# Kernel optimization log

Hardware: AMD Instinct MI355X
Metric: run time of the kernel (lower is better)

Reference implementation:

```python
import jax, jax.numpy as jnp
import numpy as np

N = 50000
E = 800000
IN_FEAT = 128
HEADS = 2
HEAD_DIM = 64  # hidden_feat // num_heads for 'concat'
HIDDEN = HEADS * HEAD_DIM
N_CLASSES = 16
NEG_SLOPE = 0.2
BN_EPS = 1e-5


def setup_inputs() -> dict:
    key = jax.random.key(0)
    ks = jax.random.split(key, 20)
    s = 0.1  # weight scale for numerical sanity
    return {
        "x": jax.random.normal(ks[0], (N, IN_FEAT), jnp.float32),
        "src0": jax.random.randint(ks[1], (E,), 0, N, jnp.int32),
        "dst0": jax.random.randint(ks[2], (E,), 0, N, jnp.int32),
        "ew0": jax.random.uniform(ks[3], (E,), jnp.float32),
        "src1": jax.random.randint(ks[4], (E,), 0, N, jnp.int32),
        "dst1": jax.random.randint(ks[5], (E,), 0, N, jnp.int32),
        "ew1": jax.random.uniform(ks[6], (E,), jnp.float32),
        "fc_w0": jax.random.normal(ks[7], (HIDDEN, IN_FEAT), jnp.float32) * s,
        "bias0": jnp.zeros((HIDDEN,), jnp.float32),
        "attn_l0": jax.random.normal(ks[8], (HEADS, HEAD_DIM), jnp.float32) * s,
        "attn_r0": jax.random.normal(ks[9], (HEADS, HEAD_DIM), jnp.float32) * s,
        "fc_w1": jax.random.normal(ks[10], (HIDDEN, IN_FEAT), jnp.float32) * s,
        "bias1": jnp.zeros((HIDDEN,), jnp.float32),
        "attn_l1": jax.random.normal(ks[11], (HEADS, HEAD_DIM), jnp.float32) * s,
        "attn_r1": jax.random.normal(ks[12], (HEADS, HEAD_DIM), jnp.float32) * s,
        "skip_w": jax.random.normal(ks[13], (HIDDEN, IN_FEAT), jnp.float32) * s,
        "skip_b": jnp.zeros((HIDDEN,), jnp.float32),
        "bn_gamma": jnp.ones((HIDDEN,), jnp.float32),
        "bn_beta": jnp.zeros((HIDDEN,), jnp.float32),
        "clf_w": jax.random.normal(ks[14], (N_CLASSES, HIDDEN), jnp.float32) * s,
        "clf_b": jnp.zeros((N_CLASSES,), jnp.float32),
    }


def _weighted_gat(x, src, dst, ew, fc_w, bias, attn_l, attn_r):
    # DGL GATConv with per-edge weight scaling of attention.
    f = (x @ fc_w.T).reshape(N, HEADS, HEAD_DIM)          # [N,H,D]
    el = jnp.sum(f * attn_l, axis=-1)                      # [N,H]
    er = jnp.sum(f * attn_r, axis=-1)                      # [N,H]
    e = jax.nn.leaky_relu(el[src] + er[dst], NEG_SLOPE)    # [E,H]
    # edge softmax over incoming edges of each dst, numerically stable
    m = jax.ops.segment_max(e, dst, num_segments=N)        # [N,H]
    ex = jnp.exp(e - m[dst])
    den = jax.ops.segment_sum(ex, dst, num_segments=N)     # [N,H]
    alpha = ex / den[dst]                                  # [E,H]
    alpha = alpha * ew[:, None]                            # edge-weight scaling
    msg = alpha[..., None] * f[src]                        # [E,H,D]
    out = jax.ops.segment_sum(msg, dst, num_segments=N)    # [N,H,D]
    return out + bias.reshape(1, HEADS, HEAD_DIM)


def reference(x, src0, dst0, ew0, src1, dst1, ew1,
              fc_w0, bias0, attn_l0, attn_r0,
              fc_w1, bias1, attn_l1, attn_r1,
              skip_w, skip_b, bn_gamma, bn_beta, clf_w, clf_b):
    # HeteroGraphConv with aggregate='sum': sum per-relation GAT outputs
    h2 = _weighted_gat(x, src0, dst0, ew0, fc_w0, bias0, attn_l0, attn_r0) \
       + _weighted_gat(x, src1, dst1, ew1, fc_w1, bias1, attn_l1, attn_r1)
    # multihead 'concat' aggregate with relu: flatten heads
    h2 = jax.nn.relu(h2).reshape(N, HIDDEN)
    # linear skip + residual add (dropout is identity at eval)
    h = (x @ skip_w.T + skip_b) + h2
    # classifier: BatchNorm1d (batch stats) -> ReLU -> Linear
    mu = jnp.mean(h, axis=0)
    var = jnp.mean((h - mu) ** 2, axis=0)
    hn = (h - mu) * jax.lax.rsqrt(var + BN_EPS) * bn_gamma + bn_beta
    logits = jax.nn.relu(hn) @ clf_w.T + clf_b
    return logits
```

## Files before the change

### kernel.cpp

```cpp
#include <hip/hip_runtime.h>
#include <hip/hip_bf16.h>

#define N_NODES 50000
#define N_EDGES 800000
#define HID 128
#define NEG_SLOPE 0.2f
#define BN_EPS 1e-5f

#define NBLK 256
#define BINSZ 512
#define BINSH 9
#define NBINS 98

typedef __bf16 v8bf __attribute__((ext_vector_type(8)));
typedef float v4f __attribute__((ext_vector_type(4)));

__device__ __forceinline__ float leaky(float v) {
    return (v > 0.f) ? v : v * NEG_SLOPE;
}
__device__ __forceinline__ unsigned int f2bu(float f) {
    __hip_bfloat16 b = __float2bfloat16(f);
    return (unsigned int)*reinterpret_cast<unsigned short*>(&b);
}
__device__ __forceinline__ unsigned int pack2bf(float lo, float hi) {
    return f2bu(lo) | (f2bu(hi) << 16);
}

__global__ __launch_bounds__(256) void k_prepw(const float* __restrict__ w0,
                                               const float* __restrict__ w1,
                                               const float* __restrict__ wsk,
                                               unsigned short* __restrict__ wb) {
    const int WQ = 128 * 128 / 4;
    int q = blockIdx.x * 256 + threadIdx.x;
    if (q >= 3 * WQ) return;
    int mat = q >> 12;
    int rem = q & 4095;
    const float* W = (mat == 0) ? w0 : (mat == 1) ? w1 : wsk;
    float4 v = ((const float4*)W)[rem];
    ushort4 o;
    o.x = (unsigned short)f2bu(v.x);
    o.y = (unsigned short)f2bu(v.y);
    o.z = (unsigned short)f2bu(v.z);
    o.w = (unsigned short)f2bu(v.w);
    *(ushort4*)(wb + (size_t)mat * 16384 + rem * 4) = o;
}

__global__ __launch_bounds__(256) void k_bincount(const int* __restrict__ dst0,
                                                  const int* __restrict__ dst1,
                                                  int* __restrict__ bincnt) {
    int rel = blockIdx.y;
    const int* dst = rel ? dst1 : dst0;
    __shared__ int cnt[NBINS];
    for (int i = threadIdx.x; i < NBINS; i += 256) cnt[i] = 0;
    __syncthreads();
    const int CH = (N_EDGES + NBLK - 1) / NBLK;
    int b0 = blockIdx.x * CH;
    int b1 = min(N_EDGES, b0 + CH);
    for (int e = b0 + threadIdx.x; e < b1; e += 256)
        atomicAdd(&cnt[dst[e] >> BINSH], 1);
    __syncthreads();
    for (int i = threadIdx.x; i < NBINS; i += 256)
        bincnt[rel * NBINS * NBLK + i * NBLK + blockIdx.x] = cnt[i];
}

__global__ __launch_bounds__(1024) void k_binscan(int* __restrict__ bincnt) {
    int* a = bincnt + blockIdx.x * NBINS * NBLK;
    const int TOT = NBINS * NBLK;
    const int CH = (TOT + 1023) / 1024;
    int tid = threadIdx.x;
    int base = tid * CH;
    int lv[CH];
    int sum = 0;
    for (int i = 0; i < CH; i++) {
        int idx = base + i;
        int v = (idx < TOT) ? a[idx] : 0;
        lv[i] = sum;
        sum += v;
    }
    __shared__ int ls[1024];
    ls[tid] = sum;
    __syncthreads();
    for (int ofs = 1; ofs < 1024; ofs <<= 1) {
        int v = (tid >= ofs) ? ls[tid - ofs] : 0;
        __syncthreads();
        ls[tid] += v;
        __syncthreads();
    }
    int pre = tid ? ls[tid - 1] : 0;
    for (int i = 0; i < CH; i++) {
        int idx = base + i;
        if (idx < TOT) a[idx] = pre + lv[i];
    }
}

__global__ __launch_bounds__(256) void k_binscatter(const int* __restrict__ dst0,
                                                    const int* __restrict__ dst1,
                                                    const int* __restrict__ src0,
                                                    const int* __restrict__ src1,
                                                    const float* __restrict__ ew0,
                                                    const float* __restrict__ ew1,
                                                    const int* __restrict__ bincnt,
                                                    int2* __restrict__ pairs0,
                                                    int2* __restrict__ pairs1) {
    int rel = blockIdx.y;
    const int* dst = rel ? dst1 : dst0;
    const int* src = rel ? src1 : src0;
    const float* ew = rel ? ew1 : ew0;
    int2* pairs = rel ? pairs1 : pairs0;
    __shared__ int cur[NBINS];
    for (int i = threadIdx.x; i < NBINS; i += 256)
        cur[i] = bincnt[rel * NBINS * NBLK + i * NBLK + blockIdx.x];
    __syncthreads();
    const int CH = (N_EDGES + NBLK - 1) / NBLK;
    int b0 = blockIdx.x * CH;
    int b1 = min(N_EDGES, b0 + CH);
    for (int e = b0 + threadIdx.x; e < b1; e += 256) {
        int d = dst[e];
        int pos = atomicAdd(&cur[d >> BINSH], 1);
        unsigned int packed = (unsigned int)(d & (BINSZ - 1)) |
                              ((unsigned int)src[e] << BINSH);
        pairs[pos] = make_int2((int)packed, __float_as_int(ew[e]));
    }
}

__global__ __launch_bounds__(256) void k_csr(const int* __restrict__ bincnt,
                                             const int2* __restrict__ pairs0,
                                             const int2* __restrict__ pairs1,
                                             const float* __restrict__ el0,
                                             const float* __restrict__ er0,
                                             const float* __restrict__ el1,
                                             const float* __restrict__ er1,
                                             int* __restrict__ offs0,
                                             int* __restrict__ offs1,
                                             int2* __restrict__ rec0,
                                             int2* __restrict__ rec1,
                                             float2* __restrict__ den20,
                                             float2* __restrict__ den21) {
    int rel = blockIdx.y;
    const int2* pairs = rel ? pairs1 : pairs0;
    const float* el = rel ? el1 : el0;
    const float* er = rel ? er1 : er0;
    int* offs = rel ? offs1 : offs0;
    int2* rec = rel ? rec1 : rec0;
    float2* den2 = rel ? den21 : den20;
    int bin = blockIdx.x;
    int tid = threadIdx.x;
    const int* bc = bincnt + rel * NBINS * NBLK;
    int pbase = bc[bin * NBLK];
    int pend = (bin < NBINS - 1) ? bc[(bin + 1) * NBLK] : N_EDGES;
    int n0 = bin << BINSH;
    int nn = min(N_NODES - n0, BINSZ);

    __shared__ int s_deg[BINSZ];
    __shared__ int s_ts[256];
    __shared__ float sden[BINSZ * 2];
    for (int i = tid; i < BINSZ; i += 256) s_deg[i] = 0;
    for (int i = tid; i < BINSZ * 2; i += 256) sden[i] = 0.f;
    __syncthreads();
    for (int p = pbase + tid; p < pend; p += 256)
        atomicAdd(&s_deg[((unsigned int)pairs[p].x) & (BINSZ - 1)], 1);
    __syncthreads();

    int d0 = s_deg[tid * 2], d1 = s_deg[tid * 2 + 1];
    s_ts[tid] = d0 + d1;
    __syncthreads();
    for (int ofs = 1; ofs < 256; ofs <<= 1) {
        int v = (tid >= ofs) ? s_ts[tid - ofs] : 0;
        __syncthreads();
        s_ts[tid] += v;
        __syncthreads();
    }
    int pre = tid ? s_ts[tid - 1] : 0;
    s_deg[tid * 2] = pbase + pre;
    s_deg[tid * 2 + 1] = pbase + pre + d0;
    __syncthreads();

    for (int l = tid; l < nn; l += 256) offs[n0 + l] = s_deg[l];
    if (bin == NBINS - 1 && tid == 0) offs[N_NODES] = N_EDGES;
    __syncthreads();

    for (int p = pbase + tid; p < pend; p += 256) {
        int2 pr = pairs[p];
        unsigned int u = (unsigned int)pr.x;
        int dl = (int)(u & (BINSZ - 1));
        int s = (int)(u >> BINSH);
        int pos = atomicAdd(&s_deg[dl], 1);
        float2 ev = *(const float2*)(el + 2 * s);
        float2 rv = *(const float2*)(er + 2 * (n0 + dl));
        float x0 = expf(leaky(ev.x + rv.x));
        float x1 = expf(leaky(ev.y + rv.y));
        atomicAdd(&sden[dl * 2], x0);
        atomicAdd(&sden[dl * 2 + 1], x1);
        float ew = __int_as_float(pr.y);
        rec[pos] = make_int2(s << 8, (int)pack2bf(x0 * ew, x1 * ew));
    }
    __syncthreads();
    for (int l = tid; l < nn; l += 256)
        den2[n0 + l] = make_float2(sden[l * 2], sden[l * 2 + 1]);
}

__global__ __launch_bounds__(256) void k_gemm_mfma(
    const float* __restrict__ x, const unsigned short* __restrict__ wb,
    const float* __restrict__ skip_b,
    const float* __restrict__ al0, const float* __restrict__ ar0,
    const float* __restrict__ al1, const float* __restrict__ ar1,
    unsigned short* __restrict__ fb0, unsigned short* __restrict__ fb1,
    float* __restrict__ el0, float* __restrict__ er0,
    float* __restrict__ el1, float* __restrict__ er1,
    float* __restrict__ hs) {
    __shared__ unsigned short As[64][128];
    __shared__ unsigned short Bs[64][128];
    int tid = threadIdx.x;
    int m0 = blockIdx.x * 64;

#pragma unroll
    for (int i = 0; i < 4; i++) {
        int idx = tid * 4 + i;
        int row = idx >> 4, seg = idx & 15;
        int gr = m0 + row;
        uint4 o = make_uint4(0, 0, 0, 0);
        if (gr < N_NODES) {
            const float* p = x + (size_t)gr * HID + seg * 8;
            float4 p0 = *(const float4*)p;
            float4 p1 = *(const float4*)(p + 4);
            o.x = pack2bf(p0.x, p0.y);
            o.y = pack2bf(p0.z, p0.w);
            o.z = pack2bf(p1.x, p1.y);
            o.w = pack2bf(p1.z, p1.w);
        }
        *(uint4*)(&As[row][(seg ^ (row & 7)) * 8]) = o;
    }
    __syncthreads();

    int w = tid >> 6, l = tid & 63;
    int lr = l & 15, lg = l >> 4;
    int node = m0 + w * 16 + lr;
    bool valid = node < N_NODES;
    int arow = w * 16 + lr;
    v8bf afrag[4];
#pragma unroll
    for (int kb = 0; kb < 4; kb++)
        afrag[kb] = *(v8bf*)(&As[arow][((kb * 4 + lg) ^ (arow & 7)) * 8]);

    for (int s = 0; s < 6; s++) {
        int mat = s >> 1;
        int j0 = (s & 1) * 64;
        const unsigned short* wmat = wb + (size_t)mat * 16384 + j0 * HID;
        __syncthreads();
#pragma unroll
        for (int i = 0; i < 4; i++) {
            int idx = tid * 4 + i;
            int row = idx >> 4, seg = idx & 15;
            uint4 wv = *(const uint4*)(wmat + row * HID + seg * 8);
            *(uint4*)(&Bs[row][(seg ^ (row & 7)) * 8]) = wv;
        }
        __syncthreads();

        v4f acc[4] = {};
#pragma unroll
        for (int nt = 0; nt < 4; nt++) {
            int brow = nt * 16 + lr;
#pragma unroll
            for (int kb = 0; kb < 4; kb++) {
                v8bf bfrag =
                    *(v8bf*)(&Bs[brow][((kb * 4 + lg) ^ (brow & 7)) * 8]);
                acc[nt] = __builtin_amdgcn_mfma_f32_16x16x32_bf16(
                    bfrag, afrag[kb], acc[nt], 0, 0, 0);
            }
        }

        if (mat < 2) {
            int h = s & 1;
            const float* al = mat ? al1 : al0;
            const float* ar = mat ? ar1 : ar0;
            float* elp = mat ? el1 : el0;
            float* erp = mat ? er1 : er0;
            unsigned short* fbp = mat ? fb1 : fb0;
            float elv = 0.f, erv = 0.f;
#pragma unroll
            for (int nt = 0; nt < 4; nt++) {
                int c0 = j0 + nt * 16 + lg * 4;
                float4 av = *(const float4*)(al + c0);
                float4 rv = *(const float4*)(ar + c0);
                elv += acc[nt][0] * av.x + acc[nt][1] * av.y +
                       acc[nt][2] * av.z + acc[nt][3] * av.w;
                erv += acc[nt][0] * rv.x + acc[nt][1] * rv.y +
                       acc[nt][2] * rv.z + acc[nt][3] * rv.w;
            }
            elv += __shfl_xor(elv, 16);
            elv += __shfl_xor(elv, 32);
            erv += __shfl_xor(erv, 16);
            erv += __shfl_xor(erv, 32);
            if (valid) {
#pragma unroll
                for (int nt = 0; nt < 4; nt++) {
                    uint2 o;
                    o.x = pack2bf(acc[nt][0], acc[nt][1]);
                    o.y = pack2bf(acc[nt][2], acc[nt][3]);
                    *(uint2*)(fbp + (size_t)node * HID + j0 + nt * 16 + lg * 4) = o;
                }
                if (lg == 0) {
                    elp[node * 2 + h] = elv;
                    erp[node * 2 + h] = erv;
                }
            }
        } else if (valid) {
#pragma unroll
            for (int nt = 0; nt < 4; nt++) {
                int c0 = j0 + nt * 16 + lg * 4;
                float4 sb = *(const float4*)(skip_b + c0);
                float4 o;
                o.x = acc[nt][0] + sb.x;
                o.y = acc[nt][1] + sb.y;
                o.z = acc[nt][2] + sb.z;
                o.w = acc[nt][3] + sb.w;
                *(float4*)(hs + (size_t)node * HID + c0) = o;
            }
        }
    }
}

__device__ __forceinline__ void agg_rel2(const int* __restrict__ offs,
                                         const int2* __restrict__ rec,
                                         const float2* __restrict__ den2,
                                         const unsigned char* __restrict__ fbb,
                                         int n, int lane, int sub,
                                         int hh, float* a) {
    int b = offs[n];
    int e_end = offs[n + 1];
    int deg = e_end - b;
    if (deg <= 0) return;
    float2 dn = den2[n];
    float inv0 = 1.f / dn.x, inv1 = 1.f / dn.y;

    int nchunk = (deg + 63) >> 6;
    for (int ch = 0; ch < nchunk; ch++) {
        int p = b + (ch << 6) + lane;
        int s = 0;
        unsigned int wpk = 0;
        if (p < e_end) {
            int2 r = rec[p];
            s = r.x;
            wpk = (unsigned int)r.y;
        }
        unsigned int pk = pack2bf(__uint_as_float(wpk << 16) * inv0,
                                  __uint_as_float(wpk & 0xffff0000u) * inv1);
        int cnt = deg - (ch << 6);
        if (cnt > 64) cnt = 64;
        int ng = (cnt + 3) >> 2;
#pragma unroll 2
        for (int g = 0; g < ng; g++) {
            int sl = (g << 2) + sub;
            int sj = __shfl(s, sl);
            unsigned int pkj = (unsigned int)__shfl((int)pk, sl);
            float aj = __uint_as_float(hh ? (pkj & 0xffff0000u) : (pkj << 16));
            uint4 fv = *(const uint4*)(fbb + sj);
            a[0] += aj * __uint_as_float(fv.x << 16);
            a[1] += aj * __uint_as_float(fv.x & 0xffff0000u);
            a[2] += aj * __uint_as_float(fv.y << 16);
            a[3] += aj * __uint_as_float(fv.y & 0xffff0000u);
            a[4] += aj * __uint_as_float(fv.z << 16);
            a[5] += aj * __uint_as_float(fv.z & 0xffff0000u);
            a[6] += aj * __uint_as_float(fv.w << 16);
            a[7] += aj * __uint_as_float(fv.w & 0xffff0000u);
        }
    }
}

__global__ __launch_bounds__(256) void k_aggregate(
    const int* __restrict__ offs0, const int2* __restrict__ rec0,
    const float2* __restrict__ den20, const unsigned short* __restrict__ fb0,
    const int* __restrict__ offs1, const int2* __restrict__ rec1,
    const float2* __restrict__ den21, const unsigned short* __restrict__ fb1,
    const float* __restrict__ bias0, const float* __restrict__ bias1,
    float* __restrict__ h) {
    int wave = threadIdx.x >> 6, lane = threadIdx.x & 63;
    int n = blockIdx.x * 4 + wave;
    if (n >= N_NODES) return;
    int cb = lane & 15;
    int sub = lane >> 4;
    int hh = cb >> 3;
    float a[8] = {0.f, 0.f, 0.f, 0.f, 0.f, 0.f, 0.f, 0.f};
    const unsigned char* fbb0 = (const unsigned char*)fb0 + cb * 16;
    const unsigned char* fbb1 = (const unsigned char*)fb1 + cb * 16;
    agg_rel2(offs0, rec0, den20, fbb0, n, lane, sub, hh, a);
    agg_rel2(offs1, rec1, den21, fbb1, n, lane, sub, hh, a);
#pragma unroll
    for (int j = 0; j < 8; j++) {
        a[j] += __shfl_xor(a[j], 16);
        a[j] += __shfl_xor(a[j], 32);
    }
    if (sub == 0) {
        size_t base = (size_t)n * HID + cb * 8;
        float4 v0 = *(const float4*)(h + base);
        float4 v1 = *(const float4*)(h + base + 4);
        int c0 = cb * 8;
        float4 o0, o1;
        o0.x = v0.x + fmaxf(a[0] + bias0[c0 + 0] + bias1[c0 + 0], 0.f);
        o0.y = v0.y + fmaxf(a[1] + bias0[c0 + 1] + bias1[c0 + 1], 0.f);
        o0.z = v0.z + fmaxf(a[2] + bias0[c0 + 2] + bias1[c0 + 2], 0.f);
        o0.w = v0.w + fmaxf(a[3] + bias0[c0 + 3] + bias1[c0 + 3], 0.f);
        o1.x = v1.x + fmaxf(a[4] + bias0[c0 + 4] + bias1[c0 + 4], 0.f);
        o1.y = v1.y + fmaxf(a[5] + bias0[c0 + 5] + bias1[c0 + 5], 0.f);
        o1.z = v1.z + fmaxf(a[6] + bias0[c0 + 6] + bias1[c0 + 6], 0.f);
        o1.w = v1.w + fmaxf(a[7] + bias0[c0 + 7] + bias1[c0 + 7], 0.f);
        *(float4*)(h + base) = o0;
        *(float4*)(h + base + 4) = o1;
    }
}

__global__ __launch_bounds__(256) void k_bnstats(const float* __restrict__ h,
                                                 double* __restrict__ psum,
                                                 double* __restrict__ psumsq) {
    int tid = threadIdx.x;
    const float4* h4 = (const float4*)h;
    double s[4] = {0.0, 0.0, 0.0, 0.0};
    double q[4] = {0.0, 0.0, 0.0, 0.0};
    const int totalv = N_NODES * HID / 4;
    const int stride = 512 * 256;
    for (int i = blockIdx.x * 256 + tid; i < totalv; i += stride) {
        float4 v = h4[i];
        s[0] += v.x; q[0] += (double)v.x * v.x;
        s[1] += v.y; q[1] += (double)v.y * v.y;
        s[2] += v.z; q[2] += (double)v.z * v.z;
        s[3] += v.w; q[3] += (double)v.w * v.w;
    }
    __shared__ double ls[256][4], lq[256][4];
#pragma unroll
    for (int j = 0; j < 4; j++) {
        ls[tid][j] = s[j];
        lq[tid][j] = q[j];
    }
    __syncthreads();
    if (tid < 32) {
#pragma unroll
        for (int j = 0; j < 4; j++) {
            double ss = 0.0, qq = 0.0;
            for (int t = tid; t < 256; t += 32) {
                ss += ls[t][j];
                qq += lq[t][j];
            }
            psum[blockIdx.x * 128 + tid * 4 + j] = ss;
            psumsq[blockIdx.x * 128 + tid * 4 + j] = qq;
        }
    }
}

__global__ void k_bn_finalize(const double* __restrict__ psum,
                              const double* __restrict__ psumsq,
                              const float* __restrict__ gamma,
                              const float* __restrict__ beta,
                              float* __restrict__ ss) {
    int c = threadIdx.x;
    double s = 0.0, q = 0.0;
    for (int b = 0; b < 512; b++) {
        s += psum[b * 128 + c];
        q += psumsq[b * 128 + c];
    }
    double mu = s / N_NODES;
    double var = q / N_NODES - mu * mu;
    float sc = gamma[c] * (float)(1.0 / sqrt(var + (double)BN_EPS));
    ss[c] = sc;
    ss[128 + c] = beta[c] - (float)mu * sc;
}

__global__ __launch_bounds__(256) void k_classify(const float* __restrict__ h,
                                                  const float* __restrict__ ss,
                                                  const float* __restrict__ clf_w,
                                                  const float* __restrict__ clf_b,
                                                  float* __restrict__ out) {
    int w = threadIdx.x >> 6, l = threadIdx.x & 63;
    int lr = l & 15, lg = l >> 4;
    int n0 = (blockIdx.x * 4 + w) * 16;
    if (n0 >= N_NODES) return;

    v8bf afrag[4], bfrag[4];
#pragma unroll
    for (int kb = 0; kb < 4; kb++) {
        int k0 = kb * 32 + lg * 8;
        const float* bp = clf_w + lr * HID + k0;
        float4 b0 = *(const float4*)bp;
        float4 b1 = *(const float4*)(bp + 4);
        bfrag[kb][0] = (__bf16)b0.x; bfrag[kb][1] = (__bf16)b0.y;
        bfrag[kb][2] = (__bf16)b0.z; bfrag[kb][3] = (__bf16)b0.w;
        bfrag[kb][4] = (__bf16)b1.x; bfrag[kb][5] = (__bf16)b1.y;
        bfrag[kb][6] = (__bf16)b1.z; bfrag[kb][7] = (__bf16)b1.w;
        const float* ap = h + (size_t)(n0 + lr) * HID + k0;
        float4 a0 = *(const float4*)ap;
        float4 a1 = *(const float4*)(ap + 4);
        float4 sc0 = *(const float4*)(ss + k0);
        float4 sc1 = *(const float4*)(ss + k0 + 4);
        float4 sh0 = *(const float4*)(ss + 128 + k0);
        float4 sh1 = *(const float4*)(ss + 128 + k0 + 4);
        afrag[kb][0] = (__bf16)fmaxf(a0.x * sc0.x + sh0.x, 0.f);
        afrag[kb][1] = (__bf16)fmaxf(a0.y * sc0.y + sh0.y, 0.f);
        afrag[kb][2] = (__bf16)fmaxf(a0.z * sc0.z + sh0.z, 0.f);
        afrag[kb][3] = (__bf16)fmaxf(a0.w * sc0.w + sh0.w, 0.f);
        afrag[kb][4] = (__bf16)fmaxf(a1.x * sc1.x + sh1.x, 0.f);
        afrag[kb][5] = (__bf16)fmaxf(a1.y * sc1.y + sh1.y, 0.f);
        afrag[kb][6] = (__bf16)fmaxf(a1.z * sc1.z + sh1.z, 0.f);
        afrag[kb][7] = (__bf16)fmaxf(a1.w * sc1.w + sh1.w, 0.f);
    }
    v4f acc = {};
#pragma unroll
    for (int kb = 0; kb < 4; kb++)
        acc = __builtin_amdgcn_mfma_f32_16x16x32_bf16(bfrag[kb], afrag[kb],
                                                      acc, 0, 0, 0);
    float4 cb = *(const float4*)(clf_b + lg * 4);
    float4 o;
    o.x = acc[0] + cb.x;
    o.y = acc[1] + cb.y;
    o.z = acc[2] + cb.z;
    o.w = acc[3] + cb.w;
    *(float4*)(out + (size_t)(n0 + lr) * 16 + lg * 4) = o;
}

extern "C" void kernel_launch(void* const* d_in, const int* in_sizes, int n_in,
                              void* d_out, int out_size, void* d_ws, size_t ws_size,
                              hipStream_t stream) {
    (void)in_sizes; (void)n_in; (void)out_size; (void)ws_size;
    const float* x      = (const float*)d_in[0];
    const int*   src0   = (const int*)d_in[1];
    const int*   dst0   = (const int*)d_in[2];
    const float* ew0    = (const float*)d_in[3];
    const int*   src1   = (const int*)d_in[4];
    const int*   dst1   = (const int*)d_in[5];
    const float* ew1    = (const float*)d_in[6];
    const float* fc_w0  = (const float*)d_in[7];
    const float* bias0  = (const float*)d_in[8];
    const float* al0    = (const float*)d_in[9];
    const float* ar0    = (const float*)d_in[10];
    const float* fc_w1  = (const float*)d_in[11];
    const float* bias1  = (const float*)d_in[12];
    const float* al1    = (const float*)d_in[13];
    const float* ar1    = (const float*)d_in[14];
    const float* skip_w = (const float*)d_in[15];
    const float* skip_b = (const float*)d_in[16];
    const float* gamma  = (const float*)d_in[17];
    const float* beta   = (const float*)d_in[18];
    const float* clf_w  = (const float*)d_in[19];
    const float* clf_b  = (const float*)d_in[20];
    float* out = (float*)d_out;

    char* wsp = (char*)d_ws;
    size_t off = 0;
    auto alloc = [&](size_t bytes) -> char* {
        char* p = wsp + off;
        off += (bytes + 255) & ~(size_t)255;
        return p;
    };
    unsigned short* wbf = (unsigned short*)alloc((size_t)3 * 16384 * 2);
    unsigned short* fb0 = (unsigned short*)alloc((size_t)N_NODES * HID * 2);
    unsigned short* fb1 = (unsigned short*)alloc((size_t)N_NODES * HID * 2);
    float*  hs     = (float*)alloc((size_t)N_NODES * HID * 4);
    float*  el0    = (float*)alloc((size_t)N_NODES * 2 * 4);
    float*  er0    = (float*)alloc((size_t)N_NODES * 2 * 4);
    float*  el1    = (float*)alloc((size_t)N_NODES * 2 * 4);
    float*  er1    = (float*)alloc((size_t)N_NODES * 2 * 4);
    int*    bincnt = (int*)alloc((size_t)2 * NBINS * NBLK * 4);
    int2*   pairs0 = (int2*)alloc((size_t)N_EDGES * 8);
    int2*   pairs1 = (int2*)alloc((size_t)N_EDGES * 8);
    int*    offs0  = (int*)alloc((size_t)(N_NODES + 1) * 4);
    int*    offs1  = (int*)alloc((size_t)(N_NODES + 1) * 4);
    int2*   rec0   = (int2*)alloc((size_t)N_EDGES * 8);
    int2*   rec1   = (int2*)alloc((size_t)N_EDGES * 8);
    float2* den20  = (float2*)alloc((size_t)N_NODES * 8);
    float2* den21  = (float2*)alloc((size_t)N_NODES * 8);
    double* psum   = (double*)alloc((size_t)512 * 128 * 8);
    double* psumsq = (double*)alloc((size_t)512 * 128 * 8);
    float*  ss     = (float*)alloc(256 * 4);

    k_prepw<<<48, 256, 0, stream>>>(fc_w0, fc_w1, skip_w, wbf);

    dim3 gbin(NBLK, 2);
    k_bincount<<<gbin, 256, 0, stream>>>(dst0, dst1, bincnt);
    k_binscan<<<2, 1024, 0, stream>>>(bincnt);
    k_binscatter<<<gbin, 256, 0, stream>>>(dst0, dst1, src0, src1, ew0, ew1,
                                           bincnt, pairs0, pairs1);

    k_gemm_mfma<<<(N_NODES + 63) / 64, 256, 0, stream>>>(
        x, wbf, skip_b, al0, ar0, al1, ar1,
        fb0, fb1, el0, er0, el1, er1, hs);

    dim3 gcsr(NBINS, 2);
    k_csr<<<gcsr, 256, 0, stream>>>(bincnt, pairs0, pairs1,
                                    el0, er0, el1, er1,
                                    offs0, offs1, rec0, rec1, den20, den21);

    k_aggregate<<<(N_NODES + 3) / 4, 256, 0, stream>>>(
        offs0, rec0, den20, fb0, offs1, rec1, den21, fb1, bias0, bias1, hs);

    k_bnstats<<<512, 256, 0, stream>>>(hs, psum, psumsq);
    k_bn_finalize<<<1, 128, 0, stream>>>(psum, psumsq, gamma, beta, ss);
    k_classify<<<(N_NODES + 63) / 64, 256, 0, stream>>>(
        hs, ss, clf_w, clf_b, out);
}
```

Before: 228.5 us.

## Merge independent kernels into shared grids to overlap scatter with GEMM

Weight conversion and bin counting now run in one launch with a block-index split. The edge bin-scatter and the MFMA GEMM also share one launch, with scatter blocks reusing the GEMM shared buffer for their cursors. This removes launch gaps and lets the memory-bound scatter run alongside the compute-bound GEMM on different CUs. The aggregation inner loop unroll is also raised from 2 to 4, which may increase register pressure.

```diff
diff --git a/kernel.cpp b/kernel.cpp
--- a/kernel.cpp
+++ b/kernel.cpp
@@ -12,6 +12,8 @@
 #define BINSH 9
 #define NBINS 98
 
+#define GEMM_BLOCKS ((N_NODES + 63) / 64)
+
 typedef __bf16 v8bf __attribute__((ext_vector_type(8)));
 typedef float v4f __attribute__((ext_vector_type(4)));
 
@@ -26,41 +28,42 @@
     return f2bu(lo) | (f2bu(hi) << 16);
 }
 
-__global__ __launch_bounds__(256) void k_prepw(const float* __restrict__ w0,
-                                               const float* __restrict__ w1,
-                                               const float* __restrict__ wsk,
-                                               unsigned short* __restrict__ wb) {
-    const int WQ = 128 * 128 / 4;
-    int q = blockIdx.x * 256 + threadIdx.x;
-    if (q >= 3 * WQ) return;
-    int mat = q >> 12;
-    int rem = q & 4095;
-    const float* W = (mat == 0) ? w0 : (mat == 1) ? w1 : wsk;
-    float4 v = ((const float4*)W)[rem];
-    ushort4 o;
-    o.x = (unsigned short)f2bu(v.x);
-    o.y = (unsigned short)f2bu(v.y);
-    o.z = (unsigned short)f2bu(v.z);
-    o.w = (unsigned short)f2bu(v.w);
-    *(ushort4*)(wb + (size_t)mat * 16384 + rem * 4) = o;
-}
-
-__global__ __launch_bounds__(256) void k_bincount(const int* __restrict__ dst0,
-                                                  const int* __restrict__ dst1,
-                                                  int* __restrict__ bincnt) {
-    int rel = blockIdx.y;
-    const int* dst = rel ? dst1 : dst0;
-    __shared__ int cnt[NBINS];
-    for (int i = threadIdx.x; i < NBINS; i += 256) cnt[i] = 0;
-    __syncthreads();
-    const int CH = (N_EDGES + NBLK - 1) / NBLK;
-    int b0 = blockIdx.x * CH;
-    int b1 = min(N_EDGES, b0 + CH);
-    for (int e = b0 + threadIdx.x; e < b1; e += 256)
-        atomicAdd(&cnt[dst[e] >> BINSH], 1);
-    __syncthreads();
-    for (int i = threadIdx.x; i < NBINS; i += 256)
-        bincnt[rel * NBINS * NBLK + i * NBLK + blockIdx.x] = cnt[i];
+__global__ __launch_bounds__(256) void k_prep_count(
+    const float* __restrict__ w0, const float* __restrict__ w1,
+    const float* __restrict__ wsk, unsigned short* __restrict__ wb,
+    const int* __restrict__ dst0, const int* __restrict__ dst1,
+    int* __restrict__ bincnt) {
+    int bid = blockIdx.x;
+    if (bid < 2 * NBLK) {
+        int rel = bid / NBLK;
+        int blk = bid % NBLK;
+        const int* dst = rel ? dst1 : dst0;
+        __shared__ int cnt[NBINS];
+        for (int i = threadIdx.x; i < NBINS; i += 256) cnt[i] = 0;
+        __syncthreads();
+        const int CH = (N_EDGES + NBLK - 1) / NBLK;
+        int b0 = blk * CH;
+        int b1 = min(N_EDGES, b0 + CH);
+        for (int e = b0 + threadIdx.x; e < b1; e += 256)
+            atomicAdd(&cnt[dst[e] >> BINSH], 1);
+        __syncthreads();
+        for (int i = threadIdx.x; i < NBINS; i += 256)
+            bincnt[rel * NBINS * NBLK + i * NBLK + blk] = cnt[i];
+    } else {
+        const int WQ = 128 * 128 / 4;
+        int q = (bid - 2 * NBLK) * 256 + threadIdx.x;
+        if (q >= 3 * WQ) return;
+        int mat = q >> 12;
+        int rem = q & 4095;
+        const float* W = (mat == 0) ? w0 : (mat == 1) ? w1 : wsk;
+        float4 v = ((const float4*)W)[rem];
+        ushort4 o;
+        o.x = (unsigned short)f2bu(v.x);
+        o.y = (unsigned short)f2bu(v.y);
+        o.z = (unsigned short)f2bu(v.z);
+        o.w = (unsigned short)f2bu(v.w);
+        *(ushort4*)(wb + (size_t)mat * 16384 + rem * 4) = o;
+    }
 }
 
 __global__ __launch_bounds__(1024) void k_binscan(int* __restrict__ bincnt) {
@@ -93,33 +96,155 @@
     }
 }
 
-__global__ __launch_bounds__(256) void k_binscatter(const int* __restrict__ dst0,
-                                                    const int* __restrict__ dst1,
-                                                    const int* __restrict__ src0,
-                                                    const int* __restrict__ src1,
-                                                    const float* __restrict__ ew0,
-                                                    const float* __restrict__ ew1,
-                                                    const int* __restrict__ bincnt,
-                                                    int2* __restrict__ pairs0,
-                                                    int2* __restrict__ pairs1) {
-    int rel = blockIdx.y;
-    const int* dst = rel ? dst1 : dst0;
-    const int* src = rel ? src1 : src0;
-    const float* ew = rel ? ew1 : ew0;
-    int2* pairs = rel ? pairs1 : pairs0;
-    __shared__ int cur[NBINS];
-    for (int i = threadIdx.x; i < NBINS; i += 256)
-        cur[i] = bincnt[rel * NBINS * NBLK + i * NBLK + blockIdx.x];
-    __syncthreads();
-    const int CH = (N_EDGES + NBLK - 1) / NBLK;
-    int b0 = blockIdx.x * CH;
-    int b1 = min(N_EDGES, b0 + CH);
-    for (int e = b0 + threadIdx.x; e < b1; e += 256) {
-        int d = dst[e];
-        int pos = atomicAdd(&cur[d >> BINSH], 1);
-        unsigned int packed = (unsigned int)(d & (BINSZ - 1)) |
-                              ((unsigned int)src[e] << BINSH);
-        pairs[pos] = make_int2((int)packed, __float_as_int(ew[e]));
+__global__ __launch_bounds__(256) void k_scatter_gemm(
+    const int* __restrict__ dst0, const int* __restrict__ dst1,
+    const int* __restrict__ src0, const int* __restrict__ src1,
+    const float* __restrict__ ew0, const float* __restrict__ ew1,
+    const int* __restrict__ bincnt,
+    int2* __restrict__ pairs0, int2* __restrict__ pairs1,
+    const float* __restrict__ x, const unsigned short* __restrict__ wb,
+    const float* __restrict__ skip_b,
+    const float* __restrict__ al0, const float* __restrict__ ar0,
+    const float* __restrict__ al1, const float* __restrict__ ar1,
+    unsigned short* __restrict__ fb0, unsigned short* __restrict__ fb1,
+    float* __restrict__ el0, float* __restrict__ er0,
+    float* __restrict__ el1, float* __restrict__ er1,
+    float* __restrict__ hs) {
+    __shared__ unsigned short As[64][128];
+    __shared__ unsigned short Bs[64][128];
+    int tid = threadIdx.x;
+    int bid = blockIdx.x;
+
+    if (bid < 2 * NBLK) {
+        int rel = bid >> 8;
+        int blk = bid & (NBLK - 1);
+        const int* dst = rel ? dst1 : dst0;
+        const int* src = rel ? src1 : src0;
+        const float* ew = rel ? ew1 : ew0;
+        int2* pairs = rel ? pairs1 : pairs0;
+        int* cur = (int*)&As[0][0];
+        for (int i = tid; i < NBINS; i += 256)
+            cur[i] = bincnt[rel * NBINS * NBLK + i * NBLK + blk];
+        __syncthreads();
+        const int CH = (N_EDGES + NBLK - 1) / NBLK;
+        int b0 = blk * CH;
+        int b1 = min(N_EDGES, b0 + CH);
+        for (int e = b0 + tid; e < b1; e += 256) {
+            int d = dst[e];
+            int pos = atomicAdd(&cur[d >> BINSH], 1);
+            unsigned int packed = (unsigned int)(d & (BINSZ - 1)) |
+                                  ((unsigned int)src[e] << BINSH);
+            pairs[pos] = make_int2((int)packed, __float_as_int(ew[e]));
+        }
+        return;
+    }
+
+    int m0 = (bid - 2 * NBLK) * 64;
+
+#pragma unroll
+    for (int i = 0; i < 4; i++) {
+        int idx = tid * 4 + i;
+        int row = idx >> 4, seg = idx & 15;
+        int gr = m0 + row;
+        uint4 o = make_uint4(0, 0, 0, 0);
+        if (gr < N_NODES) {
+            const float* p = x + (size_t)gr * HID + seg * 8;
+            float4 p0 = *(const float4*)p;
+            float4 p1 = *(const float4*)(p + 4);
+            o.x = pack2bf(p0.x, p0.y);
+            o.y = pack2bf(p0.z, p0.w);
+            o.z = pack2bf(p1.x, p1.y);
+            o.w = pack2bf(p1.z, p1.w);
+        }
+        *(uint4*)(&As[row][(seg ^ (row & 7)) * 8]) = o;
+    }
+    __syncthreads();
+
+    int w = tid >> 6, l = tid & 63;
+    int lr = l & 15, lg = l >> 4;
+    int node = m0 + w * 16 + lr;
+    bool valid = node < N_NODES;
+    int arow = w * 16 + lr;
+    v8bf afrag[4];
+#pragma unroll
+    for (int kb = 0; kb < 4; kb++)
+        afrag[kb] = *(v8bf*)(&As[arow][((kb * 4 + lg) ^ (arow & 7)) * 8]);
+
+    for (int s = 0; s < 6; s++) {
+        int mat = s >> 1;
+        int j0 = (s & 1) * 64;
+        const unsigned short* wmat = wb + (size_t)mat * 16384 + j0 * HID;
+        __syncthreads();
+#pragma unroll
+        for (int i = 0; i < 4; i++) {
+            int idx = tid * 4 + i;
+            int row = idx >> 4, seg = idx & 15;
+            uint4 wv = *(const uint4*)(wmat + row * HID + seg * 8);
+            *(uint4*)(&Bs[row][(seg ^ (row & 7)) * 8]) = wv;
+        }
+        __syncthreads();
+
+        v4f acc[4] = {};
+#pragma unroll
+        for (int nt = 0; nt < 4; nt++) {
+            int brow = nt * 16 + lr;
+#pragma unroll
+            for (int kb = 0; kb < 4; kb++) {
+                v8bf bfrag =
+                    *(v8bf*)(&Bs[brow][((kb * 4 + lg) ^ (brow & 7)) * 8]);
+                acc[nt] = __builtin_amdgcn_mfma_f32_16x16x32_bf16(
+                    bfrag, afrag[kb], acc[nt], 0, 0, 0);
+            }
+        }
+
+        if (mat < 2) {
+            int h = s & 1;
+            const float* al = mat ? al1 : al0;
+            const float* ar = mat ? ar1 : ar0;
+            float* elp = mat ? el1 : el0;
+            float* erp = mat ? er1 : er0;
+            unsigned short* fbp = mat ? fb1 : fb0;
+            float elv = 0.f, erv = 0.f;
+#pragma unroll
+            for (int nt = 0; nt < 4; nt++) {
+                int c0 = j0 + nt * 16 + lg * 4;
+                float4 av = *(const float4*)(al + c0);
+                float4 rv = *(const float4*)(ar + c0);
+                elv += acc[nt][0] * av.x + acc[nt][1] * av.y +
+                       acc[nt][2] * av.z + acc[nt][3] * av.w;
+                erv += acc[nt][0] * rv.x + acc[nt][1] * rv.y +
+                       acc[nt][2] * rv.z + acc[nt][3] * rv.w;
+            }
+            elv += __shfl_xor(elv, 16);
+            elv += __shfl_xor(elv, 32);
+            erv += __shfl_xor(erv, 16);
+            erv += __shfl_xor(erv, 32);
+            if (valid) {
+#pragma unroll
+                for (int nt = 0; nt < 4; nt++) {
+                    uint2 o;
+                    o.x = pack2bf(acc[nt][0], acc[nt][1]);
+                    o.y = pack2bf(acc[nt][2], acc[nt][3]);
+                    *(uint2*)(fbp + (size_t)node * HID + j0 + nt * 16 + lg * 4) = o;
+                }
+                if (lg == 0) {
+                    elp[node * 2 + h] = elv;
+                    erp[node * 2 + h] = erv;
+                }
+            }
+        } else if (valid) {
+#pragma unroll
+            for (int nt = 0; nt < 4; nt++) {
+                int c0 = j0 + nt * 16 + lg * 4;
+                float4 sb = *(const float4*)(skip_b + c0);
+                float4 o;
+                o.x = acc[nt][0] + sb.x;
+                o.y = acc[nt][1] + sb.y;
+                o.z = acc[nt][2] + sb.z;
+                o.w = acc[nt][3] + sb.w;
+                *(float4*)(hs + (size_t)node * HID + c0) = o;
+            }
+        }
     }
 }
 
@@ -199,127 +324,6 @@
         den2[n0 + l] = make_float2(sden[l * 2], sden[l * 2 + 1]);
 }
 
-__global__ __launch_bounds__(256) void k_gemm_mfma(
-    const float* __restrict__ x, const unsigned short* __restrict__ wb,
-    const float* __restrict__ skip_b,
-    const float* __restrict__ al0, const float* __restrict__ ar0,
-    const float* __restrict__ al1, const float* __restrict__ ar1,
-    unsigned short* __restrict__ fb0, unsigned short* __restrict__ fb1,
-    float* __restrict__ el0, float* __restrict__ er0,
-    float* __restrict__ el1, float* __restrict__ er1,
-    float* __restrict__ hs) {
-    __shared__ unsigned short As[64][128];
-    __shared__ unsigned short Bs[64][128];
-    int tid = threadIdx.x;
-    int m0 = blockIdx.x * 64;
-
-#pragma unroll
-    for (int i = 0; i < 4; i++) {
-        int idx = tid * 4 + i;
-        int row = idx >> 4, seg = idx & 15;
-        int gr = m0 + row;
-        uint4 o = make_uint4(0, 0, 0, 0);
-        if (gr < N_NODES) {
-            const float* p = x + (size_t)gr * HID + seg * 8;
-            float4 p0 = *(const float4*)p;
-            float4 p1 = *(const float4*)(p + 4);
-            o.x = pack2bf(p0.x, p0.y);
-            o.y = pack2bf(p0.z, p0.w);
-            o.z = pack2bf(p1.x, p1.y);
-            o.w = pack2bf(p1.z, p1.w);
-        }
-        *(uint4*)(&As[row][(seg ^ (row & 7)) * 8]) = o;
-    }
-    __syncthreads();
-
-    int w = tid >> 6, l = tid & 63;
-    int lr = l & 15, lg = l >> 4;
-    int node = m0 + w * 16 + lr;
-    bool valid = node < N_NODES;
-    int arow = w * 16 + lr;
-    v8bf afrag[4];
-#pragma unroll
-    for (int kb = 0; kb < 4; kb++)
-        afrag[kb] = *(v8bf*)(&As[arow][((kb * 4 + lg) ^ (arow & 7)) * 8]);
-
-    for (int s = 0; s < 6; s++) {
-        int mat = s >> 1;
-        int j0 = (s & 1) * 64;
-        const unsigned short* wmat = wb + (size_t)mat * 16384 + j0 * HID;
-        __syncthreads();
-#pragma unroll
-        for (int i = 0; i < 4; i++) {
-            int idx = tid * 4 + i;
-            int row = idx >> 4, seg = idx & 15;
-            uint4 wv = *(const uint4*)(wmat + row * HID + seg * 8);
-            *(uint4*)(&Bs[row][(seg ^ (row & 7)) * 8]) = wv;
-        }
-        __syncthreads();
-
-        v4f acc[4] = {};
-#pragma unroll
-        for (int nt = 0; nt < 4; nt++) {
-            int brow = nt * 16 + lr;
-#pragma unroll
-            for (int kb = 0; kb < 4; kb++) {
-                v8bf bfrag =
-                    *(v8bf*)(&Bs[brow][((kb * 4 + lg) ^ (brow & 7)) * 8]);
-                acc[nt] = __builtin_amdgcn_mfma_f32_16x16x32_bf16(
-                    bfrag, afrag[kb], acc[nt], 0, 0, 0);
-            }
-        }
-
-        if (mat < 2) {
-            int h = s & 1;
-            const float* al = mat ? al1 : al0;
-            const float* ar = mat ? ar1 : ar0;
-            float* elp = mat ? el1 : el0;
-            float* erp = mat ? er1 : er0;
-            unsigned short* fbp = mat ? fb1 : fb0;
-            float elv = 0.f, erv = 0.f;
-#pragma unroll
-            for (int nt = 0; nt < 4; nt++) {
-                int c0 = j0 + nt * 16 + lg * 4;
-                float4 av = *(const float4*)(al + c0);
-                float4 rv = *(const float4*)(ar + c0);
-                elv += acc[nt][0] * av.x + acc[nt][1] * av.y +
-                       acc[nt][2] * av.z + acc[nt][3] * av.w;
-                erv += acc[nt][0] * rv.x + acc[nt][1] * rv.y +
-                       acc[nt][2] * rv.z + acc[nt][3] * rv.w;
-            }
-            elv += __shfl_xor(elv, 16);
-            elv += __shfl_xor(elv, 32);
-            erv += __shfl_xor(erv, 16);
-            erv += __shfl_xor(erv, 32);
-            if (valid) {
-#pragma unroll
-                for (int nt = 0; nt < 4; nt++) {
-                    uint2 o;
-                    o.x = pack2bf(acc[nt][0], acc[nt][1]);
-                    o.y = pack2bf(acc[nt][2], acc[nt][3]);
-                    *(uint2*)(fbp + (size_t)node * HID + j0 + nt * 16 + lg * 4) = o;
-                }
-                if (lg == 0) {
-                    elp[node * 2 + h] = elv;
-                    erp[node * 2 + h] = erv;
-                }
-            }
-        } else if (valid) {
-#pragma unroll
-            for (int nt = 0; nt < 4; nt++) {
-                int c0 = j0 + nt * 16 + lg * 4;
-                float4 sb = *(const float4*)(skip_b + c0);
-                float4 o;
-                o.x = acc[nt][0] + sb.x;
-                o.y = acc[nt][1] + sb.y;
-                o.z = acc[nt][2] + sb.z;
-                o.w = acc[nt][3] + sb.w;
-                *(float4*)(hs + (size_t)node * HID + c0) = o;
-            }
-        }
-    }
-}
-
 __device__ __forceinline__ void agg_rel2(const int* __restrict__ offs,
                                          const int2* __restrict__ rec,
                                          const float2* __restrict__ den2,
@@ -348,7 +352,7 @@
         int cnt = deg - (ch << 6);
         if (cnt > 64) cnt = 64;
         int ng = (cnt + 3) >> 2;
-#pragma unroll 2
+#pragma unroll 4
         for (int g = 0; g < ng; g++) {
             int sl = (g << 2) + sub;
             int sj = __shfl(s, sl);
@@ -570,15 +574,12 @@
     double* psumsq = (double*)alloc((size_t)512 * 128 * 8);
     float*  ss     = (float*)alloc(256 * 4);
 
-    k_prepw<<<48, 256, 0, stream>>>(fc_w0, fc_w1, skip_w, wbf);
-
-    dim3 gbin(NBLK, 2);
-    k_bincount<<<gbin, 256, 0, stream>>>(dst0, dst1, bincnt);
+    k_prep_count<<<2 * NBLK + 48, 256, 0, stream>>>(fc_w0, fc_w1, skip_w, wbf,
+                                                    dst0, dst1, bincnt);
     k_binscan<<<2, 1024, 0, stream>>>(bincnt);
-    k_binscatter<<<gbin, 256, 0, stream>>>(dst0, dst1, src0, src1, ew0, ew1,
-                                           bincnt, pairs0, pairs1);
-
-    k_gemm_mfma<<<(N_NODES + 63) / 64, 256, 0, stream>>>(
+
+    k_scatter_gemm<<<2 * NBLK + GEMM_BLOCKS, 256, 0, stream>>>(
+        dst0, dst1, src0, src1, ew0, ew1, bincnt, pairs0, pairs1,
         x, wbf, skip_b, al0, ar0, al1, ar1,
         fb0, fb1, el0, er0, el1, er1, hs);
 
```

New measurement: 219.0 us. 4.2% less time.
